# Optimization experiments

Measured on AMD Instinct MI355X. Metric: run time of the kernel, lower is better.

The kernel has to match this reference:

```python
import jax, jax.numpy as jnp
import numpy as np

N_SAMPLES = 131072
N_FRAMES = 128
CPD = 16
WINDOW = 1024
N_VOICES = 8
N_BLOCKS = 3
N_CP = 512
N_VERBS = 8
MAX_ACTIVE = 32
BASE_RES = 0.5
MAX_GAIN = 5.0
B = 4
E = 16


def fft_convolve(a, b):
    # linear convolution via zero-padded rFFT, truncated to input length
    n = a.shape[-1]
    fa = jnp.fft.rfft(a, n=2 * n, axis=-1)
    fb = jnp.fft.rfft(b, n=2 * n, axis=-1)
    return jnp.fft.irfft(fa * fb, n=2 * n, axis=-1)[..., :n]


def sparsify(x, k):
    # keep top-k entries of the whole control plane, zero the rest
    flat = x.reshape(-1)
    vals, idx = jax.lax.top_k(flat, k)
    return jnp.zeros_like(flat).at[idx].set(vals).reshape(x.shape)


def run_layer(cp, w1, decays, w2, audio_map, gains):
    # cp: [CPD, F]
    frames = cp.shape[-1]
    x = w1 @ cp
    orig = x
    logd = jnp.log(1e-12 + decays)  # [CPD]
    env = jnp.exp(jnp.cumsum(jnp.broadcast_to(logd[:, None], (CPD, frames)), axis=-1))
    x = fft_convolve(x, env)
    x = w2 @ x + orig
    cp_out = jnp.tanh(x * gains[:, None])
    audio = (audio_map @ cp_out).T.reshape(-1)  # [F*WINDOW], frame-major
    return audio, cp_out


def stack_forward(cp, w1s, w2s, audios, decays_p, gains_p, mix):
    wc = cp
    outs = []
    for i in range(N_BLOCKS):
        d = BASE_RES + jax.nn.sigmoid(decays_p[i]) * (1.0 - BASE_RES)
        g = jax.nn.sigmoid(gains_p[i]) * MAX_GAIN
        out, wc = run_layer(jax.nn.relu(wc), w1s[i], d, w2s[i], audios[i], g)
        outs.append(out)
    channels = jnp.stack(outs, axis=0)  # [N_BLOCKS, N_SAMPLES]
    mixed = jnp.einsum('ct,c->t', channels, jax.nn.softmax(mix))
    return mixed / (jnp.max(jnp.abs(mixed)) + 1e-8)  # max_norm


def event_forward(voice_l, cp_choice, amp, room_l, room_mix_l, times,
                  cp_items, verbs, w1, w2, audio_maps, decays, gains, mix):
    vidx = jnp.argmax(voice_l)  # hard voice one-hot (normalize=True -> value 1.0)
    cp = cp_items[jnp.argmax(cp_choice)].reshape(CPD, N_FRAMES)
    cp = sparsify(cp / (cp.sum() + 1e-8), MAX_ACTIVE)
    samples = stack_forward(cp, w1[vidx], w2[vidx], audio_maps[vidx],
                            decays[vidx], gains[vidx], mix[vidx])  # [N_SAMPLES]
    verb = verbs[jnp.argmax(room_l)]  # hard reverb lookup
    wet = fft_convolve(verb, samples)
    vm = jax.nn.softmax(room_mix_l)  # [wet, dry]
    final = wet * vm[0] + samples * vm[1]
    final = final * jnp.abs(amp[0])
    # DiracScheduler: upsample-with-holes then FFT convolve
    step = N_SAMPLES // N_FRAMES
    impulse = jnp.zeros(N_SAMPLES, final.dtype).at[jnp.arange(N_FRAMES) * step].set(times)
    return fft_convolve(final, impulse)


def setup_inputs():
    key = jax.random.key(0)
    ks = jax.random.split(key, 14)
    return {
        'voice': jax.random.normal(ks[0], (B, E, N_VOICES), jnp.float32),
        'control_plane_choice': jax.random.normal(ks[1], (B, E, N_CP), jnp.float32),
        'amplitudes': jax.random.uniform(ks[2], (B, E, 1), jnp.float32),
        'room_choice': jax.random.normal(ks[3], (B, E, N_VERBS), jnp.float32),
        'room_mix': jax.random.normal(ks[4], (B, E, 2), jnp.float32),
        'times': jax.random.uniform(ks[5], (B, E, N_FRAMES), jnp.float32),
        'cp_items': jax.random.uniform(ks[6], (N_CP, N_FRAMES * CPD), jnp.float32),
        'verbs': jax.random.normal(ks[7], (N_VERBS, N_SAMPLES), jnp.float32) * 0.01,
        'w1': jax.random.normal(ks[8], (N_VOICES, N_BLOCKS, CPD, CPD), jnp.float32) * 0.01,
        'w2': jax.random.normal(ks[9], (N_VOICES, N_BLOCKS, CPD, CPD), jnp.float32) * 0.01,
        'audio_maps': jax.random.normal(ks[10], (N_VOICES, N_BLOCKS, WINDOW, CPD), jnp.float32) * 0.01,
        'decays': jax.random.normal(ks[11], (N_VOICES, N_BLOCKS, CPD), jnp.float32),
        'gains': jax.random.normal(ks[12], (N_VOICES, N_BLOCKS, CPD), jnp.float32),
        'mix': jax.random.normal(ks[13], (N_VOICES, N_BLOCKS), jnp.float32),
    }


def reference(voice, control_plane_choice, amplitudes, room_choice, room_mix, times,
              cp_items, verbs, w1, w2, audio_maps, decays, gains, mix):
    per_event = jax.vmap(jax.vmap(event_forward, in_axes=(0,) * 6 + (None,) * 8),
                         in_axes=(0,) * 6 + (None,) * 8)
    return per_event(voice, control_plane_choice, amplitudes, room_choice, room_mix, times,
                     cp_items, verbs, w1, w2, audio_maps, decays, gains, mix)
```

## Files before the change

### kernel.cpp

```cpp
#include <hip/hip_runtime.h>
#include <math.h>

#define NS 131072
#define NFR 128
#define CPDIM 16
#define WIN 1024
#define NVOICE 8
#define NBLK 3
#define NCP 512
#define NVERB 8
#define NEV 64
#define N1 1024
#define NBINS 1025
#define IDX(i) ((i) + ((i) >> 5))
#define VT_MAIN_BINS 1016

struct EvParams {
  int vidx, cpidx, ridx;
  float vm0, vm1, amp;
  float mixw0, mixw1, mixw2;
  unsigned int maxslot;
  int pad[6];
};

__global__ void kt_tw(float2* __restrict__ tw) {
  int k = blockIdx.x * 256 + threadIdx.x;
  if (k < 1024) {
    float ang = -3.067961575771282340e-03f * (float)k;
    float s, c;
    sincosf(ang, &s, &c);
    tw[k] = make_float2(c, s);
  }
}

__device__ __forceinline__ void fft1024(float* re, float* im,
                                        const float* twr, const float* twi,
                                        int tid, bool inverse) {
  #pragma unroll
  for (int s = 1; s <= 10; ++s) {
    const int half = 1 << (s - 1);
    const int tsh = 11 - s;
    for (int k = tid; k < 512; k += 256) {
      int j = k & (half - 1);
      int i0 = ((k ^ j) << 1) | j;
      int i1 = IDX(i0 + half);
      i0 = IDX(i0);
      float wr = twr[j << tsh];
      float wi = twi[j << tsh];
      if (inverse) wi = -wi;
      float xr = re[i1], xi = im[i1];
      float tr = wr * xr - wi * xi;
      float ti = wr * xi + wi * xr;
      float ur = re[i0], ui = im[i0];
      re[i0] = ur + tr; im[i0] = ui + ti;
      re[i1] = ur - tr; im[i1] = ui - ti;
    }
    __syncthreads();
  }
}

__device__ __forceinline__ void rfft_fwd(const float2* __restrict__ src2, float scale,
                                         float2* __restrict__ dst,
                                         float* re, float* im, float* twr, float* twi,
                                         const float2* __restrict__ twg, int tid) {
  for (int i = tid; i < 1024; i += 256) { float2 w = twg[i]; twr[i] = w.x; twi[i] = w.y; }
  for (int n = tid; n < 1024; n += 256) {
    int r = IDX(__brev(n) >> 22);
    if (n < 512) {
      float2 x = src2[n];
      re[r] = x.x * scale; im[r] = x.y * scale;
    } else { re[r] = 0.0f; im[r] = 0.0f; }
  }
  __syncthreads();
  fft1024(re, im, twr, twi, tid, false);
  for (int k = tid; k <= 1024; k += 256) {
    int km = (1024 - k) & 1023;
    float zr = re[IDX(k & 1023)], zi = im[IDX(k & 1023)];
    float mr = re[IDX(km)], mi = im[IDX(km)];
    float Are = 0.5f * (zr + mr), Aim = 0.5f * (zi - mi);
    float Bre = 0.5f * (zi + mi), Bim = 0.5f * (mr - zr);
    float wr, wi;
    if (k == 1024) { wr = -1.0f; wi = 0.0f; }
    else { wr = twr[k]; wi = twi[k]; }
    dst[k] = make_float2(Are + wr * Bre - wi * Bim, Aim + wr * Bim + wi * Bre);
  }
}

template<int NROWS>
__device__ __forceinline__ void fft512_rows(float* re, float* im,
                                            const float* twr, const float* twi,
                                            int tid) {
  #pragma unroll
  for (int s = 1; s <= 9; ++s) {
    const int half = 1 << (s - 1);
    const int tsh = 9 - s;
    for (int q = tid; q < NROWS * 256; q += 256) {
      int row = q >> 8, k = q & 255;
      int j = k & (half - 1);
      int i0 = ((k ^ j) << 1) | j;
      int a0 = row * 513 + i0, a1 = a0 + half;
      float wr = twr[j << tsh];
      float wi = twi[j << tsh];
      float xr = re[a1], xi = im[a1];
      float tr = wr * xr - wi * xi;
      float ti = wr * xi + wi * xr;
      float ur = re[a0], ui = im[a0];
      re[a0] = ur + tr; im[a0] = ui + ti;
      re[a1] = ur - tr; im[a1] = ui - ti;
    }
    __syncthreads();
  }
}

template<int NROWS>
__device__ __forceinline__ void ifft512_rows_dif(float* re, float* im,
                                                 const float* twr, const float* twi,
                                                 int tid) {
  #pragma unroll
  for (int s = 9; s >= 1; --s) {
    const int half = 1 << (s - 1);
    const int tsh = 9 - s;
    for (int q = tid; q < NROWS * 256; q += 256) {
      int row = q >> 8, k = q & 255;
      int j = k & (half - 1);
      int i0 = ((k ^ j) << 1) | j;
      int a0 = row * 513 + i0, a1 = a0 + half;
      float wr = twr[j << tsh];
      float wi = -twi[j << tsh];
      float ur = re[a0], ui = im[a0];
      float vr = re[a1], vi = im[a1];
      re[a0] = ur + vr; im[a0] = ui + vi;
      float dr = ur - vr, di = ui - vi;
      re[a1] = dr * wr - di * wi;
      im[a1] = dr * wi + di * wr;
    }
    __syncthreads();
  }
}

__global__ void k0_params(const float* __restrict__ voice, const float* __restrict__ cpc,
                          const float* __restrict__ amps, const float* __restrict__ roomc,
                          const float* __restrict__ roomm, const float* __restrict__ mix,
                          EvParams* __restrict__ P) {
  int e = blockIdx.x;
  int tid = threadIdx.x;
  __shared__ float bvals[64];
  __shared__ int bidx[64];

  if (tid == 0) {
    const float* v = voice + e * NVOICE;
    int vi = 0; float bv = v[0];
    for (int i = 1; i < NVOICE; ++i) if (v[i] > bv) { bv = v[i]; vi = i; }
    P[e].vidx = vi;

    const float* r = roomc + e * NVERB;
    int ri = 0; float br = r[0];
    for (int i = 1; i < NVERB; ++i) if (r[i] > br) { br = r[i]; ri = i; }
    P[e].ridx = ri;

    float m0 = roomm[e * 2 + 0], m1 = roomm[e * 2 + 1];
    float mx = fmaxf(m0, m1);
    float e0 = expf(m0 - mx), e1 = expf(m1 - mx);
    float inv = 1.0f / (e0 + e1);
    P[e].vm0 = e0 * inv;
    P[e].vm1 = e1 * inv;
    P[e].amp = fabsf(amps[e]);

    const float* mm = mix + vi * NBLK;
    float mmx = fmaxf(fmaxf(mm[0], mm[1]), mm[2]);
    float w0 = expf(mm[0] - mmx), w1 = expf(mm[1] - mmx), w2 = expf(mm[2] - mmx);
    float si = 1.0f / (w0 + w1 + w2);
    P[e].mixw0 = w0 * si; P[e].mixw1 = w1 * si; P[e].mixw2 = w2 * si;
    P[e].maxslot = 0u;
  }

  const float* c = cpc + (size_t)e * NCP;
  float bv = -INFINITY; int bi = 0;
  for (int i = tid; i < NCP; i += 64) {
    float x = c[i];
    if (x > bv) { bv = x; bi = i; }
  }
  bvals[tid] = bv; bidx[tid] = bi;
  __syncthreads();
  if (tid == 0) {
    float best = bvals[0]; int besti = bidx[0];
    for (int i = 1; i < 64; ++i) {
      if (bvals[i] > best || (bvals[i] == best && bidx[i] < besti)) { best = bvals[i]; besti = bidx[i]; }
    }
    P[e].cpidx = besti;
  }
}

__global__ __launch_bounds__(256) void kv_fft(const float* __restrict__ verbs,
                                              const float2* __restrict__ twg,
                                              float2* __restrict__ Vhat) {
  __shared__ float re[N1 + 32], im[N1 + 32];
  __shared__ float twr[N1], twi[N1];
  int v = blockIdx.x >> 7, j = blockIdx.x & 127;
  int tid = threadIdx.x;
  rfft_fwd((const float2*)(verbs + (size_t)v * NS + j * WIN), 1.0f,
           Vhat + ((size_t)v * NFR + j) * NBINS, re, im, twr, twi, twg, tid);
}

__global__ __launch_bounds__(256) void kv2_cfft(const float2* __restrict__ Vhat,
                                                const float2* __restrict__ twg,
                                                float2* __restrict__ VtMain,
                                                float2* __restrict__ VtRest) {
  __shared__ float zre[8 * 513], zim[8 * 513];
  __shared__ float twr[256], twi[256];
  int v = blockIdx.x / 129, bg = blockIdx.x % 129;
  int b0 = bg * 8;
  int tid = threadIdx.x;
  { float2 w = twg[4 * tid]; twr[tid] = w.x; twi[tid] = w.y; }
  const float2* Vg = Vhat + (size_t)v * NFR * NBINS;
  for (int idx = tid; idx < 1024; idx += 256) {
    int p = idx >> 3, bb = idx & 7;
    int bin = b0 + bb; if (bin > 1024) bin = 1024;
    float2 x = Vg[p * NBINS + bin];
    int r = __brev(p) >> 23;
    zre[bb * 513 + r] = x.x; zim[bb * 513 + r] = x.y;
  }
  for (int idx = tid; idx < 3072; idx += 256) {
    int p = 128 + (idx >> 3), bb = idx & 7;
    int r = __brev(p) >> 23;
    zre[bb * 513 + r] = 0.f; zim[bb * 513 + r] = 0.f;
  }
  __syncthreads();
  fft512_rows<8>(zre, zim, twr, twi, tid);
  for (int idx = tid; idx < 4096; idx += 256) {
    int bb = idx >> 9, c = idx & 511;
    int bin = b0 + bb;
    if (bin <= 1024) {
      float2 val = make_float2(zre[bb * 513 + c], zim[bb * 513 + c]);
      if (bin < VT_MAIN_BINS) VtMain[((size_t)v * VT_MAIN_BINS + bin) * 512 + c] = val;
      else VtRest[((size_t)v * 9 + (bin - VT_MAIN_BINS)) * 512 + c] = val;
    }
  }
}

__global__ __launch_bounds__(256) void kt_times(const float* __restrict__ times_g,
                                                const float2* __restrict__ twg,
                                                float2* __restrict__ That) {
  __shared__ float re[513], im[513];
  __shared__ float twr[256], twi[256];
  int e = blockIdx.x, tid = threadIdx.x;
  { float2 w = twg[4 * tid]; twr[tid] = w.x; twi[tid] = w.y; }
  for (int p = tid; p < 512; p += 256) {
    int r = __brev(p) >> 23;
    float v = (p < 128) ? times_g[e * NFR + p] : 0.f;
    re[r] = v; im[r] = 0.f;
  }
  __syncthreads();
  fft512_rows<1>(re, im, twr, twi, tid);
  for (int c = tid; c < 512; c += 256) That[(size_t)e * 512 + c] = make_float2(re[c], im[c]);
}

__global__ __launch_bounds__(256) void k1a_synth(const float* __restrict__ cp_items,
                                                 const float* __restrict__ w1_all,
                                                 const float* __restrict__ w2_all,
                                                 const float* __restrict__ decays,
                                                 const float* __restrict__ gains,
                                                 const EvParams* __restrict__ P,
                                                 float* __restrict__ cp_out_all) {
  __shared__ float wc[2048], xb[2048], yb[2048];
  __shared__ float w1s[256], w2s[256];
  __shared__ float dv[16], gv[16];
  __shared__ float rv[4];
  __shared__ int ri[4];
  __shared__ float s_scale;

  int e = blockIdx.x, tid = threadIdx.x;
  int vidx = P[e].vidx, cpidx = P[e].cpidx;
  int base = tid * 8;

  float vals[8];
  float ls = 0.0f;
  #pragma unroll
  for (int q = 0; q < 8; ++q) {
    float x = cp_items[(size_t)cpidx * 2048 + base + q];
    vals[q] = x; ls += x;
  }
  #pragma unroll
  for (int off = 32; off > 0; off >>= 1) ls += __shfl_xor(ls, off);
  if ((tid & 63) == 0) rv[tid >> 6] = ls;
  __syncthreads();
  if (tid == 0) s_scale = 1.0f / (rv[0] + rv[1] + rv[2] + rv[3] + 1e-8f);
  for (int i = tid; i < 2048; i += 256) wc[i] = 0.0f;
  __syncthreads();
  float scale = s_scale;

  for (int it = 0; it < 32; ++it) {
    float bv = -1.0f; int bi = 1 << 30;
    #pragma unroll
    for (int q = 0; q < 8; ++q) {
      if (vals[q] > bv) { bv = vals[q]; bi = base + q; }
    }
    #pragma unroll
    for (int off = 32; off > 0; off >>= 1) {
      float ov = __shfl_xor(bv, off); int oi = __shfl_xor(bi, off);
      if (ov > bv || (ov == bv && oi < bi)) { bv = ov; bi = oi; }
    }
    if ((tid & 63) == 0) { rv[tid >> 6] = bv; ri[tid >> 6] = bi; }
    __syncthreads();
    float wv = rv[0]; int wi = ri[0];
    #pragma unroll
    for (int w = 1; w < 4; ++w) {
      if (rv[w] > wv || (rv[w] == wv && ri[w] < wi)) { wv = rv[w]; wi = ri[w]; }
    }
    if ((wi >> 3) == tid) { vals[wi & 7] = -2.0f; wc[wi] = wv * scale; }
    __syncthreads();
  }

  for (int l = 0; l < NBLK; ++l) {
    int wbase = (vidx * NBLK + l) * 256;
    w1s[tid] = w1_all[wbase + tid];
    w2s[tid] = w2_all[wbase + tid];
    if (tid < 16) {
      float dp = decays[(vidx * NBLK + l) * 16 + tid];
      float sd = 1.0f / (1.0f + expf(-dp));
      dv[tid] = 1e-12f + 0.5f + 0.5f * sd;
      float gp = gains[(vidx * NBLK + l) * 16 + tid];
      gv[tid] = 5.0f / (1.0f + expf(-gp));
    }
    __syncthreads();
    for (int i = tid; i < 2048; i += 256) {
      int cch = i >> 7, f = i & 127;
      float acc = 0.0f;
      #pragma unroll
      for (int k = 0; k < 16; ++k) acc += w1s[cch * 16 + k] * fmaxf(wc[k * 128 + f], 0.0f);
      xb[i] = acc;
    }
    __syncthreads();
    if (tid < 16) {
      float a = 0.0f, d = dv[tid];
      for (int t = 0; t < 128; ++t) { a = d * (a + xb[tid * 128 + t]); yb[tid * 128 + t] = a; }
    }
    __syncthreads();
    for (int i = tid; i < 2048; i += 256) {
      int cch = i >> 7, f = i & 127;
      float acc = xb[i];
      #pragma unroll
      for (int k = 0; k < 16; ++k) acc += w2s[cch * 16 + k] * yb[k * 128 + f];
      float co = tanhf(acc * gv[cch]);
      wc[i] = co;
      cp_out_all[((size_t)e * NBLK + l) * 2048 + i] = co;
    }
    __syncthreads();
  }
}

__global__ __launch_bounds__(256) void k1b_audio(const float* __restrict__ amaps,
                                                 const float* __restrict__ cp_out_all,
                                                 EvParams* __restrict__ P,
                                                 float* __restrict__ mixed) {
  __shared__ float cps[NBLK][16][16];
  __shared__ float red[256];
  int e = blockIdx.x >> 3, fg = blockIdx.x & 7;
  int f0 = fg * 16, tid = threadIdx.x;
  int vidx = P[e].vidx;
  float mw[3] = {P[e].mixw0, P[e].mixw1, P[e].mixw2};

  for (int i = tid; i < NBLK * 256; i += 256) {
    int bl = i >> 8, r = i & 255, cch = r >> 4, fl = r & 15;
    cps[bl][cch][fl] = cp_out_all[((size_t)e * NBLK + bl) * 2048 + cch * 128 + f0 + fl];
  }
  __syncthreads();

  float amax = 0.0f;
  for (int jw = 0; jw < 4; ++jw) {
    int w = jw * 256 + tid;
    float am[NBLK][16];
    #pragma unroll
    for (int bl = 0; bl < NBLK; ++bl) {
      const float* ap = amaps + (((size_t)(vidx * NBLK + bl)) * WIN + w) * CPDIM;
      #pragma unroll
      for (int cch = 0; cch < 16; ++cch) am[bl][cch] = ap[cch] * mw[bl];
    }
    for (int fl = 0; fl < 16; ++fl) {
      float acc = 0.0f;
      #pragma unroll
      for (int bl = 0; bl < NBLK; ++bl)
        #pragma unroll
        for (int cch = 0; cch < 16; ++cch) acc += am[bl][cch] * cps[bl][cch][fl];
      mixed[(size_t)e * NS + (size_t)(f0 + fl) * WIN + w] = acc;
      amax = fmaxf(amax, fabsf(acc));
    }
  }
  red[tid] = amax;
  __syncthreads();
  for (int s = 128; s > 0; s >>= 1) { if (tid < s) red[tid] = fmaxf(red[tid], red[tid + s]); __syncthreads(); }
  if (tid == 0) atomicMax(&P[e].maxslot, __float_as_uint(red[0]));
}

__global__ __launch_bounds__(256) void k2_fwd(const float* __restrict__ mixed,
                                              const float2* __restrict__ twg,
                                              float2* __restrict__ Shat) {
  __shared__ float re[N1 + 32], im[N1 + 32];
  __shared__ float twr[N1], twi[N1];
  int e = blockIdx.x >> 7, p = blockIdx.x & 127;
  int tid = threadIdx.x;
  rfft_fwd((const float2*)(mixed + (size_t)e * NS + p * WIN), 1.0f,
           Shat + ((size_t)e * NFR + p) * NBINS, re, im, twr, twi, twg, tid);
}

__global__ __launch_bounds__(256) void k3_fft(float2* __restrict__ Shat,
                                              const float2* __restrict__ VtMain,
                                              const float2* __restrict__ VtRest,
                                              const float2* __restrict__ That,
                                              const float2* __restrict__ twg,
                                              const EvParams* __restrict__ P) {
  __shared__ float zre[8 * 513], zim[8 * 513];
  __shared__ float twr[256], twi[256];
  int e = blockIdx.x / 129, bg = blockIdx.x % 129;
  int b0 = bg * 8;
  int tid = threadIdx.x;
  int ridx = P[e].ridx;
  float vm0 = P[e].vm0, vm1 = P[e].vm1;
  float ampn = P[e].amp / (__uint_as_float(P[e].maxslot) + 1e-8f) * (1.0f / 512.0f);
  { float2 w = twg[4 * tid]; twr[tid] = w.x; twi[tid] = w.y; }

  float2* Sg = Shat + (size_t)e * NFR * NBINS;
  for (int idx = tid; idx < 1024; idx += 256) {
    int p = idx >> 3, bb = idx & 7;
    int bin = b0 + bb; if (bin > 1024) bin = 1024;
    float2 x = Sg[p * NBINS + bin];
    int r = __brev(p) >> 23;
    zre[bb * 513 + r] = x.x; zim[bb * 513 + r] = x.y;
  }
  for (int idx = tid; idx < 3072; idx += 256) {
    int p = 128 + (idx >> 3), bb = idx & 7;
    int r = __brev(p) >> 23;
    zre[bb * 513 + r] = 0.f; zim[bb * 513 + r] = 0.f;
  }
  __syncthreads();
  fft512_rows<8>(zre, zim, twr, twi, tid);

  for (int idx = tid; idx < 4096; idx += 256) {
    int bb = idx >> 9, c = idx & 511;
    int bin = b0 + bb; if (bin > 1024) bin = 1024;
    float2 V = (bin < VT_MAIN_BINS) ? VtMain[((size_t)ridx * VT_MAIN_BINS + bin) * 512 + c]
                                    : VtRest[((size_t)ridx * 9 + (bin - VT_MAIN_BINS)) * 512 + c];
    float2 T = That[(size_t)e * 512 + c];
    float wr0 = vm0 * V.x + vm1, wi0 = vm0 * V.y;
    float wr = (wr0 * T.x - wi0 * T.y) * ampn;
    float wi = (wr0 * T.y + wi0 * T.x) * ampn;
    float zr = zre[bb * 513 + c], zi = zim[bb * 513 + c];
    zre[bb * 513 + c] = zr * wr - zi * wi;
    zim[bb * 513 + c] = zr * wi + zi * wr;
  }
  __syncthreads();
  ifft512_rows_dif<8>(zre, zim, twr, twi, tid);

  for (int idx = tid; idx < 1024; idx += 256) {
    int p = idx >> 3, bb = idx & 7;
    int bin = b0 + bb;
    int r = __brev(p) >> 23;
    if (bin <= 1024) Sg[p * NBINS + bin] = make_float2(zre[bb * 513 + r], zim[bb * 513 + r]);
  }
}

__global__ __launch_bounds__(256) void k4_ifft(const float2* __restrict__ Ohat,
                                               const float2* __restrict__ twg,
                                               float* __restrict__ out,
                                               float* __restrict__ tail) {
  __shared__ float re[N1 + 32], im[N1 + 32];
  __shared__ float twr[N1], twi[N1];
  int e = blockIdx.x >> 7, p = blockIdx.x & 127;
  int tid = threadIdx.x;
  const float2* src = Ohat + ((size_t)e * NFR + p) * NBINS;
  for (int i = tid; i < 1024; i += 256) { float2 w = twg[i]; twr[i] = w.x; twi[i] = w.y; }
  __syncthreads();
  for (int k = tid; k < 1024; k += 256) {
    float2 Xk = src[k];
    float2 Xm = src[1024 - k];
    float Are = 0.5f * (Xk.x + Xm.x), Aim = 0.5f * (Xk.y - Xm.y);
    float Dre = 0.5f * (Xk.x - Xm.x), Dim = 0.5f * (Xk.y + Xm.y);
    float wr = twr[k], wi = twi[k];
    float Bre = wr * Dre + wi * Dim;
    float Bim = wr * Dim - wi * Dre;
    int r = IDX(__brev(k) >> 22);
    re[r] = Are - Bim;
    im[r] = Aim + Bre;
  }
  __syncthreads();
  fft1024(re, im, twr, twi, tid, true);
  const float inv = 1.0f / (float)N1;
  float2* o2 = (float2*)(out + (size_t)e * NS + (size_t)p * WIN);
  for (int n = tid; n < 512; n += 256) o2[n] = make_float2(re[IDX(n)] * inv, im[IDX(n)] * inv);
  float2* t2 = (float2*)(tail + ((size_t)e * NFR + p) * WIN);
  for (int n = tid; n < 512; n += 256) t2[n] = make_float2(re[IDX(n + 512)] * inv, im[IDX(n + 512)] * inv);
}

__global__ __launch_bounds__(256) void k5_tail(const float* __restrict__ tail, float* __restrict__ out) {
  size_t idx = (size_t)blockIdx.x * 256 + threadIdx.x;
  if (idx >= (size_t)NEV * 127 * WIN) return;
  int u = (int)(idx & 1023);
  size_t rest = idx >> 10;
  int pm1 = (int)(rest % 127);
  int e = (int)(rest / 127);
  int p = pm1 + 1;
  out[(size_t)e * NS + (size_t)p * WIN + u] += tail[((size_t)e * NFR + pm1) * WIN + u];
}

extern "C" void kernel_launch(void* const* d_in, const int* in_sizes, int n_in,
                              void* d_out, int out_size, void* d_ws, size_t ws_size,
                              hipStream_t stream) {
  (void)in_sizes; (void)n_in; (void)out_size; (void)ws_size;
  const float* voice    = (const float*)d_in[0];
  const float* cpc      = (const float*)d_in[1];
  const float* amps     = (const float*)d_in[2];
  const float* roomc    = (const float*)d_in[3];
  const float* roomm    = (const float*)d_in[4];
  const float* times    = (const float*)d_in[5];
  const float* cp_items = (const float*)d_in[6];
  const float* verbs    = (const float*)d_in[7];
  const float* w1       = (const float*)d_in[8];
  const float* w2       = (const float*)d_in[9];
  const float* amaps    = (const float*)d_in[10];
  const float* decays   = (const float*)d_in[11];
  const float* gains    = (const float*)d_in[12];
  const float* mix      = (const float*)d_in[13];
  float* out = (float*)d_out;

  char* base = (char*)d_ws;
  EvParams* P       = (EvParams*)base;
  float2* twg       = (float2*)(base + 4096);
  float* cp_out_all = (float*)(base + 4096 + 8192);
  float* mixed      = cp_out_all + (size_t)393216;
  float2* Shat      = (float2*)(mixed + (size_t)8388608);
  float2* Vhat      = Shat + (size_t)NEV * NFR * NBINS;
  float2* That      = (float2*)cp_out_all;
  float2* VtRest    = (float2*)((char*)cp_out_all + 262144);
  float2* VtMain    = (float2*)out;
  float* tail  = mixed;
  float2* Ohat = Shat;

  kt_tw<<<4, 256, 0, stream>>>(twg);
  k0_params<<<NEV, 64, 0, stream>>>(voice, cpc, amps, roomc, roomm, mix, P);
  kv_fft<<<NVERB * NFR, 256, 0, stream>>>(verbs, twg, Vhat);
  k1a_synth<<<NEV, 256, 0, stream>>>(cp_items, w1, w2, decays, gains, P, cp_out_all);
  k1b_audio<<<NEV * 8, 256, 0, stream>>>(amaps, cp_out_all, P, mixed);
  kv2_cfft<<<NVERB * 129, 256, 0, stream>>>(Vhat, twg, VtMain, VtRest);
  kt_times<<<NEV, 256, 0, stream>>>(times, twg, That);
  k2_fwd<<<NEV * NFR, 256, 0, stream>>>(mixed, twg, Shat);
  k3_fft<<<NEV * 129, 256, 0, stream>>>(Shat, VtMain, VtRest, That, twg, P);
  k4_ifft<<<NEV * NFR, 256, 0, stream>>>(Ohat, twg, out, tail);
  k5_tail<<<(NEV * 127 * WIN) / 256, 256, 0, stream>>>(tail, out);
}
```

Before: 672.9 us.

## Replace shared-memory 512-point FFTs with register/wave-shuffle FFTs in frame-axis kernels

The 512-point frame-axis FFTs in the reverb-spectrum, times and main convolution kernels now run one wavefront per row. Each lane holds 8 points in registers, the first three stages run inside the register set, and the last six use cross-lane shuffles. Twiddles come from per-lane sincospi, and the forward transform skips the known-zero upper 3/4 of the input. This removes the nine __syncthreads-separated LDS passes per FFT and the bit-reversal scatter. The costs are higher register pressure, the loss of the shared twiddle table, and a different ordering of the output bins that the twiddle and multiply code must match.

```diff
diff --git a/kernel.cpp b/kernel.cpp
--- a/kernel.cpp
+++ b/kernel.cpp
@@ -22,6 +22,13 @@
   unsigned int maxslot;
   int pad[6];
 };
+
+__device__ __forceinline__ float2 cmul(float2 a, float2 b) {
+  return make_float2(a.x * b.x - a.y * b.y, a.x * b.y + a.y * b.x);
+}
+__device__ __forceinline__ float2 cadd(float2 a, float2 b) { return make_float2(a.x + b.x, a.y + b.y); }
+__device__ __forceinline__ float2 csub(float2 a, float2 b) { return make_float2(a.x - b.x, a.y - b.y); }
+__device__ __forceinline__ float2 cconj(float2 a) { return make_float2(a.x, -a.y); }
 
 __global__ void kt_tw(float2* __restrict__ tw) {
   int k = blockIdx.x * 256 + threadIdx.x;
@@ -86,55 +93,112 @@
   }
 }
 
-template<int NROWS>
-__device__ __forceinline__ void fft512_rows(float* re, float* im,
-                                            const float* twr, const float* twi,
-                                            int tid) {
-  #pragma unroll
-  for (int s = 1; s <= 9; ++s) {
-    const int half = 1 << (s - 1);
-    const int tsh = 9 - s;
-    for (int q = tid; q < NROWS * 256; q += 256) {
-      int row = q >> 8, k = q & 255;
-      int j = k & (half - 1);
-      int i0 = ((k ^ j) << 1) | j;
-      int a0 = row * 513 + i0, a1 = a0 + half;
-      float wr = twr[j << tsh];
-      float wi = twi[j << tsh];
-      float xr = re[a1], xi = im[a1];
-      float tr = wr * xr - wi * xi;
-      float ti = wr * xi + wi * xr;
-      float ur = re[a0], ui = im[a0];
-      re[a0] = ur + tr; im[a0] = ui + ti;
-      re[a1] = ur - tr; im[a1] = ui - ti;
-    }
-    __syncthreads();
-  }
-}
-
-template<int NROWS>
-__device__ __forceinline__ void ifft512_rows_dif(float* re, float* im,
-                                                 const float* twr, const float* twi,
-                                                 int tid) {
-  #pragma unroll
-  for (int s = 9; s >= 1; --s) {
-    const int half = 1 << (s - 1);
-    const int tsh = 9 - s;
-    for (int q = tid; q < NROWS * 256; q += 256) {
-      int row = q >> 8, k = q & 255;
-      int j = k & (half - 1);
-      int i0 = ((k ^ j) << 1) | j;
-      int a0 = row * 513 + i0, a1 = a0 + half;
-      float wr = twr[j << tsh];
-      float wi = -twi[j << tsh];
-      float ur = re[a0], ui = im[a0];
-      float vr = re[a1], vi = im[a1];
-      re[a0] = ur + vr; im[a0] = ui + vi;
-      float dr = ur - vr, di = ui - vi;
-      re[a1] = dr * wr - di * wi;
-      im[a1] = dr * wi + di * wr;
-    }
-    __syncthreads();
+struct Tw512 {
+  float2 b64, t128_0, t128_1, t256_0, t256_1, t256_2, t256_3, t32, t16, t8, t4, t2;
+};
+
+__device__ __forceinline__ float2 eneg(float frac) {
+  float s, c; sincospif(frac, &s, &c); return make_float2(c, -s);
+}
+
+__device__ __forceinline__ Tw512 mk_tw512(int lane) {
+  const float C = 0.70710678118654752f;
+  Tw512 t;
+  t.b64 = eneg((float)lane * (1.0f / 64.0f));
+  float2 b128 = eneg((float)lane * (1.0f / 128.0f));
+  t.t128_0 = b128;
+  t.t128_1 = make_float2(b128.y, -b128.x);
+  float2 b256 = eneg((float)lane * (1.0f / 256.0f));
+  t.t256_0 = b256;
+  t.t256_1 = cmul(b256, make_float2(C, -C));
+  t.t256_2 = make_float2(b256.y, -b256.x);
+  t.t256_3 = cmul(b256, make_float2(-C, -C));
+  t.t32 = eneg((float)(lane & 31) * (1.0f / 32.0f));
+  t.t16 = eneg((float)(lane & 15) * (1.0f / 16.0f));
+  t.t8  = eneg((float)(lane & 7)  * (1.0f / 8.0f));
+  int j4 = lane & 3;
+  t.t4 = (j4 == 0) ? make_float2(1.f, 0.f) : (j4 == 1) ? make_float2(C, -C)
+       : (j4 == 2) ? make_float2(0.f, -1.f) : make_float2(-C, -C);
+  t.t2 = (lane & 1) ? make_float2(0.f, -1.f) : make_float2(1.f, 0.f);
+  return t;
+}
+
+__device__ __forceinline__ void fwd_sh(float2* x, int h, float2 t, int lane) {
+  bool hi = (lane & h) != 0;
+  #pragma unroll
+  for (int r = 0; r < 8; ++r) {
+    float yr = __shfl_xor(x[r].x, h);
+    float yi = __shfl_xor(x[r].y, h);
+    float2 s = make_float2(x[r].x + yr, x[r].y + yi);
+    float2 d = cmul(make_float2(yr - x[r].x, yi - x[r].y), t);
+    x[r] = hi ? d : s;
+  }
+}
+
+__device__ __forceinline__ void inv_sh(float2* x, int h, float2 tc, int lane) {
+  bool hi = (lane & h) != 0;
+  #pragma unroll
+  for (int r = 0; r < 8; ++r) {
+    float2 z = hi ? cmul(x[r], tc) : x[r];
+    float zr = __shfl_xor(z.x, h);
+    float zi = __shfl_xor(z.y, h);
+    x[r] = hi ? make_float2(zr - z.x, zi - z.y) : make_float2(z.x + zr, z.y + zi);
+  }
+}
+
+__device__ __forceinline__ void fft512_fwd(float2* x, const Tw512& T, int lane) {
+  {
+    float2 u, v;
+    u = x[0]; v = x[4]; x[0] = cadd(u, v); x[4] = cmul(csub(u, v), T.t256_0);
+    u = x[1]; v = x[5]; x[1] = cadd(u, v); x[5] = cmul(csub(u, v), T.t256_1);
+    u = x[2]; v = x[6]; x[2] = cadd(u, v); x[6] = cmul(csub(u, v), T.t256_2);
+    u = x[3]; v = x[7]; x[3] = cadd(u, v); x[7] = cmul(csub(u, v), T.t256_3);
+  }
+  {
+    float2 u, v;
+    u = x[0]; v = x[2]; x[0] = cadd(u, v); x[2] = cmul(csub(u, v), T.t128_0);
+    u = x[1]; v = x[3]; x[1] = cadd(u, v); x[3] = cmul(csub(u, v), T.t128_1);
+    u = x[4]; v = x[6]; x[4] = cadd(u, v); x[6] = cmul(csub(u, v), T.t128_0);
+    u = x[5]; v = x[7]; x[5] = cadd(u, v); x[7] = cmul(csub(u, v), T.t128_1);
+  }
+  #pragma unroll
+  for (int r = 0; r < 8; r += 2) {
+    float2 u = x[r], v = x[r + 1];
+    x[r] = cadd(u, v); x[r + 1] = cmul(csub(u, v), T.b64);
+  }
+  fwd_sh(x, 32, T.t32, lane);
+  fwd_sh(x, 16, T.t16, lane);
+  fwd_sh(x, 8,  T.t8,  lane);
+  fwd_sh(x, 4,  T.t4,  lane);
+  fwd_sh(x, 2,  T.t2,  lane);
+  fwd_sh(x, 1,  make_float2(1.f, 0.f), lane);
+}
+
+__device__ __forceinline__ void fft512_inv(float2* x, const Tw512& T, int lane) {
+  inv_sh(x, 1,  make_float2(1.f, 0.f), lane);
+  inv_sh(x, 2,  cconj(T.t2),  lane);
+  inv_sh(x, 4,  cconj(T.t4),  lane);
+  inv_sh(x, 8,  cconj(T.t8),  lane);
+  inv_sh(x, 16, cconj(T.t16), lane);
+  inv_sh(x, 32, cconj(T.t32), lane);
+  #pragma unroll
+  for (int r = 0; r < 8; r += 2) {
+    float2 u = x[r], v = cmul(x[r + 1], cconj(T.b64));
+    x[r] = cadd(u, v); x[r + 1] = csub(u, v);
+  }
+  {
+    float2 u, v;
+    u = x[0]; v = cmul(x[2], cconj(T.t128_0)); x[0] = cadd(u, v); x[2] = csub(u, v);
+    u = x[1]; v = cmul(x[3], cconj(T.t128_1)); x[1] = cadd(u, v); x[3] = csub(u, v);
+    u = x[4]; v = cmul(x[6], cconj(T.t128_0)); x[4] = cadd(u, v); x[6] = csub(u, v);
+    u = x[5]; v = cmul(x[7], cconj(T.t128_1)); x[5] = cadd(u, v); x[7] = csub(u, v);
+  }
+  {
+    float2 u, v;
+    u = x[0]; v = cmul(x[4], cconj(T.t256_0)); x[0] = cadd(u, v); x[4] = csub(u, v);
+    u = x[1]; v = cmul(x[5], cconj(T.t256_1)); x[1] = cadd(u, v); x[5] = csub(u, v);
+    u = x[2]; v = cmul(x[6], cconj(T.t256_2)); x[2] = cadd(u, v); x[6] = csub(u, v);
+    u = x[3]; v = cmul(x[7], cconj(T.t256_3)); x[3] = cadd(u, v); x[7] = csub(u, v);
   }
 }
 
@@ -202,57 +266,52 @@
            Vhat + ((size_t)v * NFR + j) * NBINS, re, im, twr, twi, twg, tid);
 }
 
-__global__ __launch_bounds__(256) void kv2_cfft(const float2* __restrict__ Vhat,
-                                                const float2* __restrict__ twg,
-                                                float2* __restrict__ VtMain,
-                                                float2* __restrict__ VtRest) {
-  __shared__ float zre[8 * 513], zim[8 * 513];
-  __shared__ float twr[256], twi[256];
+__global__ __launch_bounds__(256) void kv2_reg(const float2* __restrict__ Vhat,
+                                               float2* __restrict__ VtMain,
+                                               float2* __restrict__ VtRest) {
+  __shared__ float2 tile[8][132];
   int v = blockIdx.x / 129, bg = blockIdx.x % 129;
   int b0 = bg * 8;
-  int tid = threadIdx.x;
-  { float2 w = twg[4 * tid]; twr[tid] = w.x; twi[tid] = w.y; }
+  int tid = threadIdx.x, lane = tid & 63, w = tid >> 6;
+
   const float2* Vg = Vhat + (size_t)v * NFR * NBINS;
   for (int idx = tid; idx < 1024; idx += 256) {
     int p = idx >> 3, bb = idx & 7;
     int bin = b0 + bb; if (bin > 1024) bin = 1024;
-    float2 x = Vg[p * NBINS + bin];
-    int r = __brev(p) >> 23;
-    zre[bb * 513 + r] = x.x; zim[bb * 513 + r] = x.y;
-  }
-  for (int idx = tid; idx < 3072; idx += 256) {
-    int p = 128 + (idx >> 3), bb = idx & 7;
-    int r = __brev(p) >> 23;
-    zre[bb * 513 + r] = 0.f; zim[bb * 513 + r] = 0.f;
-  }
-  __syncthreads();
-  fft512_rows<8>(zre, zim, twr, twi, tid);
-  for (int idx = tid; idx < 4096; idx += 256) {
-    int bb = idx >> 9, c = idx & 511;
+    tile[bb][p] = Vg[p * NBINS + bin];
+  }
+  __syncthreads();
+
+  Tw512 T = mk_tw512(lane);
+  for (int q = 0; q < 2; ++q) {
+    int bb = w * 2 + q;
     int bin = b0 + bb;
-    if (bin <= 1024) {
-      float2 val = make_float2(zre[bb * 513 + c], zim[bb * 513 + c]);
-      if (bin < VT_MAIN_BINS) VtMain[((size_t)v * VT_MAIN_BINS + bin) * 512 + c] = val;
-      else VtRest[((size_t)v * 9 + (bin - VT_MAIN_BINS)) * 512 + c] = val;
-    }
-  }
-}
-
-__global__ __launch_bounds__(256) void kt_times(const float* __restrict__ times_g,
-                                                const float2* __restrict__ twg,
-                                                float2* __restrict__ That) {
-  __shared__ float re[513], im[513];
-  __shared__ float twr[256], twi[256];
-  int e = blockIdx.x, tid = threadIdx.x;
-  { float2 w = twg[4 * tid]; twr[tid] = w.x; twi[tid] = w.y; }
-  for (int p = tid; p < 512; p += 256) {
-    int r = __brev(p) >> 23;
-    float v = (p < 128) ? times_g[e * NFR + p] : 0.f;
-    re[r] = v; im[r] = 0.f;
-  }
-  __syncthreads();
-  fft512_rows<1>(re, im, twr, twi, tid);
-  for (int c = tid; c < 512; c += 256) That[(size_t)e * 512 + c] = make_float2(re[c], im[c]);
+    if (bin > 1024) continue;
+    float2 xx[8];
+    xx[0] = tile[bb][lane];
+    xx[1] = tile[bb][64 + lane];
+    #pragma unroll
+    for (int r = 2; r < 8; ++r) xx[r] = make_float2(0.f, 0.f);
+    fft512_fwd(xx, T, lane);
+    float2* dst = (bin < VT_MAIN_BINS) ? (VtMain + ((size_t)v * VT_MAIN_BINS + bin) * 512)
+                                       : (VtRest + ((size_t)v * 9 + (bin - VT_MAIN_BINS)) * 512);
+    #pragma unroll
+    for (int r = 0; r < 8; ++r) dst[64 * r + lane] = xx[r];
+  }
+}
+
+__global__ __launch_bounds__(64) void kt_reg(const float* __restrict__ times_g,
+                                             float2* __restrict__ That) {
+  int e = blockIdx.x, lane = threadIdx.x;
+  Tw512 T = mk_tw512(lane);
+  float2 xx[8];
+  xx[0] = make_float2(times_g[e * NFR + lane], 0.f);
+  xx[1] = make_float2(times_g[e * NFR + 64 + lane], 0.f);
+  #pragma unroll
+  for (int r = 2; r < 8; ++r) xx[r] = make_float2(0.f, 0.f);
+  fft512_fwd(xx, T, lane);
+  #pragma unroll
+  for (int r = 0; r < 8; ++r) That[(size_t)e * 512 + 64 * r + lane] = xx[r];
 }
 
 __global__ __launch_bounds__(256) void k1a_synth(const float* __restrict__ cp_items,
@@ -403,59 +462,64 @@
            Shat + ((size_t)e * NFR + p) * NBINS, re, im, twr, twi, twg, tid);
 }
 
-__global__ __launch_bounds__(256) void k3_fft(float2* __restrict__ Shat,
+__global__ __launch_bounds__(256) void k3_reg(float2* __restrict__ Shat,
                                               const float2* __restrict__ VtMain,
                                               const float2* __restrict__ VtRest,
                                               const float2* __restrict__ That,
-                                              const float2* __restrict__ twg,
                                               const EvParams* __restrict__ P) {
-  __shared__ float zre[8 * 513], zim[8 * 513];
-  __shared__ float twr[256], twi[256];
+  __shared__ float2 tile[8][132];
   int e = blockIdx.x / 129, bg = blockIdx.x % 129;
   int b0 = bg * 8;
-  int tid = threadIdx.x;
+  int tid = threadIdx.x, lane = tid & 63, w = tid >> 6;
   int ridx = P[e].ridx;
   float vm0 = P[e].vm0, vm1 = P[e].vm1;
   float ampn = P[e].amp / (__uint_as_float(P[e].maxslot) + 1e-8f) * (1.0f / 512.0f);
-  { float2 w = twg[4 * tid]; twr[tid] = w.x; twi[tid] = w.y; }
 
   float2* Sg = Shat + (size_t)e * NFR * NBINS;
   for (int idx = tid; idx < 1024; idx += 256) {
     int p = idx >> 3, bb = idx & 7;
     int bin = b0 + bb; if (bin > 1024) bin = 1024;
-    float2 x = Sg[p * NBINS + bin];
-    int r = __brev(p) >> 23;
-    zre[bb * 513 + r] = x.x; zim[bb * 513 + r] = x.y;
-  }
-  for (int idx = tid; idx < 3072; idx += 256) {
-    int p = 128 + (idx >> 3), bb = idx & 7;
-    int r = __brev(p) >> 23;
-    zre[bb * 513 + r] = 0.f; zim[bb * 513 + r] = 0.f;
-  }
-  __syncthreads();
-  fft512_rows<8>(zre, zim, twr, twi, tid);
-
-  for (int idx = tid; idx < 4096; idx += 256) {
-    int bb = idx >> 9, c = idx & 511;
-    int bin = b0 + bb; if (bin > 1024) bin = 1024;
-    float2 V = (bin < VT_MAIN_BINS) ? VtMain[((size_t)ridx * VT_MAIN_BINS + bin) * 512 + c]
-                                    : VtRest[((size_t)ridx * 9 + (bin - VT_MAIN_BINS)) * 512 + c];
-    float2 T = That[(size_t)e * 512 + c];
-    float wr0 = vm0 * V.x + vm1, wi0 = vm0 * V.y;
-    float wr = (wr0 * T.x - wi0 * T.y) * ampn;
-    float wi = (wr0 * T.y + wi0 * T.x) * ampn;
-    float zr = zre[bb * 513 + c], zi = zim[bb * 513 + c];
-    zre[bb * 513 + c] = zr * wr - zi * wi;
-    zim[bb * 513 + c] = zr * wi + zi * wr;
-  }
-  __syncthreads();
-  ifft512_rows_dif<8>(zre, zim, twr, twi, tid);
+    tile[bb][p] = Sg[p * NBINS + bin];
+  }
+  __syncthreads();
+
+  Tw512 T = mk_tw512(lane);
+  const float2* Trow = That + (size_t)e * 512;
+
+  for (int q = 0; q < 2; ++q) {
+    int bb = w * 2 + q;
+    int bin = b0 + bb;
+    int binc = bin > 1024 ? 1024 : bin;
+    float2 xx[8];
+    xx[0] = tile[bb][lane];
+    xx[1] = tile[bb][64 + lane];
+    #pragma unroll
+    for (int r = 2; r < 8; ++r) xx[r] = make_float2(0.f, 0.f);
+    fft512_fwd(xx, T, lane);
+
+    const float2* Vrow = (binc < VT_MAIN_BINS) ? (VtMain + ((size_t)ridx * VT_MAIN_BINS + binc) * 512)
+                                               : (VtRest + ((size_t)ridx * 9 + (binc - VT_MAIN_BINS)) * 512);
+    #pragma unroll
+    for (int r = 0; r < 8; ++r) {
+      int n = 64 * r + lane;
+      float2 V = Vrow[n];
+      float2 Tt = Trow[n];
+      float2 wv = make_float2(vm0 * V.x + vm1, vm0 * V.y);
+      float2 wt = cmul(wv, Tt);
+      wt.x *= ampn; wt.y *= ampn;
+      xx[r] = cmul(xx[r], wt);
+    }
+
+    fft512_inv(xx, T, lane);
+    tile[bb][lane] = xx[0];
+    tile[bb][64 + lane] = xx[1];
+  }
+  __syncthreads();
 
   for (int idx = tid; idx < 1024; idx += 256) {
     int p = idx >> 3, bb = idx & 7;
     int bin = b0 + bb;
-    int r = __brev(p) >> 23;
-    if (bin <= 1024) Sg[p * NBINS + bin] = make_float2(zre[bb * 513 + r], zim[bb * 513 + r]);
+    if (bin <= 1024) Sg[p * NBINS + bin] = tile[bb][p];
   }
 }
 
@@ -540,10 +604,10 @@
   kv_fft<<<NVERB * NFR, 256, 0, stream>>>(verbs, twg, Vhat);
   k1a_synth<<<NEV, 256, 0, stream>>>(cp_items, w1, w2, decays, gains, P, cp_out_all);
   k1b_audio<<<NEV * 8, 256, 0, stream>>>(amaps, cp_out_all, P, mixed);
-  kv2_cfft<<<NVERB * 129, 256, 0, stream>>>(Vhat, twg, VtMain, VtRest);
-  kt_times<<<NEV, 256, 0, stream>>>(times, twg, That);
+  kv2_reg<<<NVERB * 129, 256, 0, stream>>>(Vhat, VtMain, VtRest);
+  kt_reg<<<NEV, 64, 0, stream>>>(times, That);
   k2_fwd<<<NEV * NFR, 256, 0, stream>>>(mixed, twg, Shat);
-  k3_fft<<<NEV * 129, 256, 0, stream>>>(Shat, VtMain, VtRest, That, twg, P);
+  k3_reg<<<NEV * 129, 256, 0, stream>>>(Shat, VtMain, VtRest, That, P);
   k4_ifft<<<NEV * NFR, 256, 0, stream>>>(Ohat, twg, out, tail);
   k5_tail<<<(NEV * 127 * WIN) / 256, 256, 0, stream>>>(tail, out);
 }
```

Measured after the change: 580.2 us. 13.8% less time.
